# Kernel tuning notes

Measured on AMD Instinct MI355X. Metric: run time of the kernel, lower is better.

The kernel has to match this reference:

```python
import jax, jax.numpy as jnp
import numpy as np

WS = 7   # window size (square)
SS = 3   # shift size
NH = 4   # num heads


def build_rel_index(ws):
    # relative_position_index, identical to the torch buffer construction
    coords = np.stack(np.meshgrid(np.arange(ws), np.arange(ws), indexing='ij'))  # (2, ws, ws)
    flat = coords.reshape(2, -1)                       # (2, ws*ws)
    rel = flat[:, :, None] - flat[:, None, :]          # (2, N, N)
    rel = rel.transpose(1, 2, 0).copy()                # (N, N, 2)
    rel[:, :, 0] += ws - 1
    rel[:, :, 1] += ws - 1
    rel[:, :, 0] *= 2 * ws - 1
    return rel.sum(-1)                                 # (N, N) int


def build_shift_mask(Hp, Wp, ws, ss):
    # additive mask (nW, N, N) with 0 / -100, same as compute_mask
    img = np.zeros((Hp, Wp))
    cnt = 0
    for hs in (slice(0, -ws), slice(-ws, -ss), slice(-ss, None)):
        for wsl in (slice(0, -ws), slice(-ws, -ss), slice(-ss, None)):
            img[hs, wsl] = cnt
            cnt += 1
    mw = img.reshape(Hp // ws, ws, Wp // ws, ws).transpose(0, 2, 1, 3).reshape(-1, ws * ws)
    diff = mw[:, None, :] - mw[:, :, None]
    return jnp.asarray(np.where(diff != 0, -100.0, 0.0).astype(np.float32))


def setup_inputs() -> dict:
    key = jax.random.key(0)
    k1, k2, k3, k4 = jax.random.split(key, 4)
    B, H, W, C = 32, 56, 56, 128
    x = jax.random.normal(k1, (B, H, W, C), dtype=jnp.float32)
    rpb_table = jax.random.normal(k2, ((2 * WS - 1) * (2 * WS - 1), NH), dtype=jnp.float32) * 0.02
    w_qkv = jax.random.normal(k3, (3 * C, C), dtype=jnp.float32) * 0.02
    w_proj = jax.random.normal(k4, (C, C), dtype=jnp.float32) * 0.02
    b_proj = jnp.zeros((C,), dtype=jnp.float32)
    return {"x": x, "rpb_table": rpb_table, "w_qkv": w_qkv, "w_proj": w_proj, "b_proj": b_proj}


def reference(x, rpb_table, w_qkv, w_proj, b_proj):
    B, H, W, C = x.shape
    hd = C // NH
    scale = hd ** (-0.5)
    # pad to multiples of window (no-op for 56x56 / 7)
    pad_b = (-H) % WS
    pad_r = (-W) % WS
    x = jnp.pad(x, ((0, 0), (0, pad_b), (0, pad_r), (0, 0)))
    Hp, Wp = H + pad_b, W + pad_r
    # cyclic shift
    xs = jnp.roll(x, (-SS, -SS), axis=(1, 2))
    nWh, nWw = Hp // WS, Wp // WS
    N = WS * WS
    nW = nWh * nWw
    # window partition -> (B*nW, N, C)
    win = xs.reshape(B, nWh, WS, nWw, WS, C).transpose(0, 1, 3, 2, 4, 5).reshape(-1, N, C)
    # qkv projection (no bias)
    qkv = (win @ w_qkv.T).reshape(-1, N, 3, NH, hd)
    q = qkv[:, :, 0].transpose(0, 2, 1, 3) * scale   # (B_, NH, N, hd)
    k = qkv[:, :, 1].transpose(0, 2, 1, 3)
    v = qkv[:, :, 2].transpose(0, 2, 1, 3)
    attn = jnp.einsum('bhid,bhjd->bhij', q, k)       # (B_, NH, N, N)
    # relative position bias gather
    rel_idx = build_rel_index(WS)                    # (N, N) static
    bias = rpb_table[rel_idx.reshape(-1)].reshape(N, N, NH).transpose(2, 0, 1)
    attn = attn + bias[None]
    # shift mask (shift > 0 since H,W > window)
    mask = build_shift_mask(Hp, Wp, WS, SS)          # (nW, N, N)
    attn = attn.reshape(B, nW, NH, N, N) + mask[None, :, None]
    attn = jax.nn.softmax(attn.reshape(-1, NH, N, N), axis=-1)
    out = jnp.einsum('bhij,bhjd->bihd', attn, v).reshape(-1, N, C)
    out = out @ w_proj.T + b_proj
    # window reverse (square windows -> equivalent to torch code)
    out = out.reshape(B, nWh, nWw, WS, WS, C).transpose(0, 1, 3, 2, 4, 5).reshape(B, Hp, Wp, C)
    out = jnp.roll(out, (SS, SS), axis=(1, 2))
    return out[:, :H, :W, :]
```

## Files before the change

### kernel.cpp

```cpp
#include <hip/hip_runtime.h>


#define HWD 56
#define SCALE_Q 0.17677669529663687f

typedef _Float16 f16x8 __attribute__((ext_vector_type(8)));
typedef __fp16   h16x2 __attribute__((ext_vector_type(2)));
typedef float    f32x4 __attribute__((ext_vector_type(4)));

__device__ __forceinline__ unsigned pkrtz(float a, float b) {
    union { h16x2 h; unsigned u; } r;
    r.h = __builtin_amdgcn_cvt_pkrtz(a, b);
    return r.u;
}

__device__ __forceinline__ f32x4 mfma16(const unsigned a[4], const unsigned b[4], f32x4 c) {
    union { unsigned u[4]; f16x8 h; } A, B;
    A.u[0] = a[0]; A.u[1] = a[1]; A.u[2] = a[2]; A.u[3] = a[3];
    B.u[0] = b[0]; B.u[1] = b[1]; B.u[2] = b[2]; B.u[3] = b[3];
    return __builtin_amdgcn_mfma_f32_16x16x32_f16(A.h, B.h, c, 0, 0, 0);
}

__device__ __forceinline__ unsigned short f16b(float v) {
    union { _Float16 h; unsigned short s; } cv; cv.h = (_Float16)v; return cv.s;
}

__global__ void prep2(const float* __restrict__ rpb,
                      const float* __restrict__ w_qkv,
                      const float* __restrict__ w_proj,
                      unsigned short* __restrict__ whQKV,
                      unsigned short* __restrict__ whP,
                      float* __restrict__ biasT)
{
    int idx = blockIdx.x * 256 + threadIdx.x;
    if (idx < 49152) {
        float v = w_qkv[idx];
        if (idx < 16384) v *= SCALE_Q;
        whQKV[idx] = f16b(v);
    } else if (idx < 65536) {
        int j = idx - 49152;
        whP[j] = f16b(w_proj[j]);
    } else {
        int k = idx - 65536;
        int j = k & 63, i = (k >> 6) & 63, h = (k >> 12) & 3, t = k >> 14;
        float v;
        if (j >= 49)      v = -1e30f;
        else if (i >= 49) v = 0.f;
        else {
            int ri = i / 7, ci = i % 7, rj = j / 7, cj = j % 7;
            int rel = (ri - rj + 6) * 13 + (ci - cj + 6);
            v = rpb[rel * 4 + h];
            int gi = ((t & 2) ? (ri < 4 ? 1 : 2) : 0) * 3 + ((t & 1) ? (ci < 4 ? 1 : 2) : 0);
            int gj = ((t & 2) ? (rj < 4 ? 1 : 2) : 0) * 3 + ((t & 1) ? (cj < 4 ? 1 : 2) : 0);
            if (gi != gj) v -= 100.f;
        }
        biasT[k] = v;
    }
}

__global__ __launch_bounds__(256, 3)
void swin_msa_mfma6(const float* __restrict__ x,
                    const unsigned short* __restrict__ whQKV,
                    const unsigned short* __restrict__ whP,
                    const float* __restrict__ b_proj,
                    const float* __restrict__ biasT,
                    float* __restrict__ out)
{
    __shared__ __align__(16) unsigned short Xs[64 * 136];
    __shared__ __align__(16) unsigned short Osh[64 * 136];

    const int tid  = threadIdx.x;
    const int h    = tid >> 6;
    const int lane = tid & 63;
    const int c    = lane & 15;
    const int g    = lane >> 4;

    const int blk  = blockIdx.x;
    const int b    = blk >> 6;
    const int wIdx = blk & 63;
    const int wh   = wIdx >> 3, ww = wIdx & 7;
    const int wtype = ((wh == 7) ? 2 : 0) | ((ww == 7) ? 1 : 0);

    auto tokAddr = [&](int tok) {
        int rr = tok / 7, cc = tok - rr * 7;
        int sh = wh * 7 + rr + 3; if (sh >= HWD) sh -= HWD;
        int sw = ww * 7 + cc + 3; if (sw >= HWD) sw -= HWD;
        return ((b * HWD + sh) * HWD + sw) * 128;
    };

    for (int idx = tid; idx < 2048; idx += 256) {
        int tok = idx >> 5, ch4 = (idx & 31) << 2;
        uint2 wv = make_uint2(0u, 0u);
        if (tok < 49) {
            const float4 v = *(const float4*)(x + tokAddr(tok) + ch4);
            wv = make_uint2(pkrtz(v.x, v.y), pkrtz(v.z, v.w));
        }
        *(uint2*)&Xs[tok * 136 + ch4] = wv;
    }
    __syncthreads();

    const int srcA  = c | ((lane & 16) << 1);
    const int srcB  = srcA + 16;
    const bool hiSel = (lane & 32) != 0;

    auto redist = [&](const unsigned pkLo[2], const unsigned pkHi[2], unsigned f[4]) {
        #pragma unroll
        for (int p = 0; p < 2; ++p) {
            unsigned lo0 = __shfl(pkLo[p], srcA);
            unsigned hi0 = __shfl(pkHi[p], srcA);
            f[p] = hiSel ? hi0 : lo0;
            unsigned lo1 = __shfl(pkLo[p], srcB);
            unsigned hi1 = __shfl(pkHi[p], srcB);
            f[2 + p] = hiSel ? hi1 : lo1;
        }
    };
    auto loadW = [&](const unsigned short* wbase, int rowBase, unsigned af[4][4]) {
        const unsigned short* wr = wbase + (rowBase + c) * 128 + g * 8;
        #pragma unroll
        for (int kk = 0; kk < 4; ++kk) {
            uint4 v = *(const uint4*)(wr + kk * 32);
            af[kk][0] = v.x; af[kk][1] = v.y; af[kk][2] = v.z; af[kk][3] = v.w;
        }
    };
    auto xfrag = [&](int nt, unsigned xB[4][4]) {
        const unsigned short* xr = &Xs[(nt * 16 + c) * 136 + g * 8];
        #pragma unroll
        for (int kk = 0; kk < 4; ++kk) {
            uint4 v = *(const uint4*)(xr + kk * 32);
            xB[kk][0] = v.x; xB[kk][1] = v.y; xB[kk][2] = v.z; xB[kk][3] = v.w;
        }
    };

    unsigned qB[4][4];
    unsigned kA[4][4];
    unsigned vA[2][2][4];
    {
        unsigned pkP[2][4][2];
        #pragma unroll
        for (int ql = 0; ql < 2; ++ql) {
            unsigned af[4][4];
            loadW(whQKV, 32 * h + 16 * ql, af);
            #pragma unroll
            for (int nt = 0; nt < 4; ++nt) {
                unsigned xB[4][4]; xfrag(nt, xB);
                f32x4 acc = {0.f, 0.f, 0.f, 0.f};
                #pragma unroll
                for (int kk = 0; kk < 4; ++kk) acc = mfma16(af[kk], xB[kk], acc);
                pkP[ql][nt][0] = pkrtz(acc[0], acc[1]);
                pkP[ql][nt][1] = pkrtz(acc[2], acc[3]);
            }
        }
        #pragma unroll
        for (int nt = 0; nt < 4; ++nt) redist(pkP[0][nt], pkP[1][nt], qB[nt]);

        #pragma unroll
        for (int kl = 0; kl < 2; ++kl) {
            unsigned af[4][4];
            loadW(whQKV, 128 + 32 * h + 16 * kl, af);
            #pragma unroll
            for (int mt = 0; mt < 4; ++mt) {
                unsigned xB[4][4]; xfrag(mt, xB);
                f32x4 acc = {0.f, 0.f, 0.f, 0.f};
                #pragma unroll
                for (int kk = 0; kk < 4; ++kk) acc = mfma16(af[kk], xB[kk], acc);
                pkP[kl][mt][0] = pkrtz(acc[0], acc[1]);
                pkP[kl][mt][1] = pkrtz(acc[2], acc[3]);
            }
        }
        #pragma unroll
        for (int mt = 0; mt < 4; ++mt) redist(pkP[0][mt], pkP[1][mt], kA[mt]);
    }
    #pragma unroll
    for (int vl = 0; vl < 2; ++vl) {
        unsigned bf[4][4];
        loadW(whQKV, 256 + 32 * h + 16 * vl, bf);
        unsigned pkV[4][2];
        #pragma unroll
        for (int mt = 0; mt < 4; ++mt) {
            unsigned xA[4][4]; xfrag(mt, xA);
            f32x4 acc = {0.f, 0.f, 0.f, 0.f};
            #pragma unroll
            for (int kk = 0; kk < 4; ++kk) acc = mfma16(xA[kk], bf[kk], acc);
            pkV[mt][0] = pkrtz(acc[0], acc[1]);
            pkV[mt][1] = pkrtz(acc[2], acc[3]);
        }
        #pragma unroll
        for (int kv = 0; kv < 2; ++kv)
            redist(pkV[2 * kv], pkV[2 * kv + 1], vA[vl][kv]);
    }

    const float* bT = biasT + (wtype * 4 + h) * 4096;

    #pragma unroll
    for (int nt = 0; nt < 4; ++nt) {
        f32x4 S[4];
        #pragma unroll
        for (int mt = 0; mt < 4; ++mt) {
            float4 b4 = *(const float4*)&bT[(nt * 16 + c) * 64 + mt * 16 + 4 * g];
            f32x4 C = { b4.x, b4.y, b4.z, b4.w };
            S[mt] = mfma16(kA[mt], qB[nt], C);
        }
        float m = -1e30f;
        #pragma unroll
        for (int mt = 0; mt < 4; ++mt)
            #pragma unroll
            for (int r = 0; r < 4; ++r) m = fmaxf(m, S[mt][r]);
        m = fmaxf(m, __shfl_xor(m, 16));
        m = fmaxf(m, __shfl_xor(m, 32));
        float s = 0.f;
        #pragma unroll
        for (int mt = 0; mt < 4; ++mt)
            #pragma unroll
            for (int r = 0; r < 4; ++r) { float e = __expf(S[mt][r] - m); S[mt][r] = e; s += e; }
        s += __shfl_xor(s, 16);
        s += __shfl_xor(s, 32);
        const float iv = 1.0f / s;

        f32x4 o0 = {0.f, 0.f, 0.f, 0.f};
        f32x4 o1 = {0.f, 0.f, 0.f, 0.f};
        #pragma unroll
        for (int kk = 0; kk < 2; ++kk) {
            unsigned pkLo[2], pkHi[2];
            pkLo[0] = pkrtz(S[2 * kk][0] * iv,     S[2 * kk][1] * iv);
            pkLo[1] = pkrtz(S[2 * kk][2] * iv,     S[2 * kk][3] * iv);
            pkHi[0] = pkrtz(S[2 * kk + 1][0] * iv, S[2 * kk + 1][1] * iv);
            pkHi[1] = pkrtz(S[2 * kk + 1][2] * iv, S[2 * kk + 1][3] * iv);
            unsigned pB[4];
            redist(pkLo, pkHi, pB);
            o0 = mfma16(vA[0][kk], pB, o0);
            o1 = mfma16(vA[1][kk], pB, o1);
        }
        *(uint2*)&Osh[(nt * 16 + c) * 136 + 32 * h + 4 * g] =
            make_uint2(pkrtz(o0[0], o0[1]), pkrtz(o0[2], o0[3]));
        *(uint2*)&Osh[(nt * 16 + c) * 136 + 32 * h + 16 + 4 * g] =
            make_uint2(pkrtz(o1[0], o1[1]), pkrtz(o1[2], o1[3]));
    }
    __syncthreads();

    int taddr[4];
    #pragma unroll
    for (int nt = 0; nt < 4; ++nt) {
        int tok = nt * 16 + c;
        taddr[nt] = (tok < 49) ? tokAddr(tok) : -1;
    }
    unsigned oB[4][4][4];
    #pragma unroll
    for (int nt = 0; nt < 4; ++nt)
        #pragma unroll
        for (int kk = 0; kk < 4; ++kk) {
            uint4 v = *(const uint4*)&Osh[(nt * 16 + c) * 136 + kk * 32 + g * 8];
            oB[nt][kk][0] = v.x; oB[nt][kk][1] = v.y; oB[nt][kk][2] = v.z; oB[nt][kk][3] = v.w;
        }
    #pragma unroll
    for (int mi = 0; mi < 2; ++mi) {
        const int mt = 2 * h + mi;
        unsigned aW[4][4];
        loadW(whP, 16 * mt, aW);
        float4 bias4 = *(const float4*)(b_proj + mt * 16 + 4 * g);
        #pragma unroll
        for (int nt = 0; nt < 4; ++nt) {
            f32x4 acc = {0.f, 0.f, 0.f, 0.f};
            #pragma unroll
            for (int kk = 0; kk < 4; ++kk) acc = mfma16(aW[kk], oB[nt][kk], acc);
            if (taddr[nt] >= 0) {
                float4 o = make_float4(acc[0] + bias4.x, acc[1] + bias4.y,
                                       acc[2] + bias4.z, acc[3] + bias4.w);
                *(float4*)(out + taddr[nt] + mt * 16 + 4 * g) = o;
            }
        }
    }
}

extern "C" void kernel_launch(void* const* d_in, const int* in_sizes, int n_in,
                              void* d_out, int out_size, void* d_ws, size_t ws_size,
                              hipStream_t stream) {
    const float* x     = (const float*)d_in[0];
    const float* rpb   = (const float*)d_in[1];
    const float* wqkv  = (const float*)d_in[2];
    const float* wproj = (const float*)d_in[3];
    const float* bproj = (const float*)d_in[4];
    float* outp = (float*)d_out;

    unsigned short* whQKV = (unsigned short*)d_ws;
    unsigned short* whP   = whQKV + 49152;
    float* biasT = (float*)(whP + 16384);

    prep2<<<512, 256, 0, stream>>>(rpb, wqkv, wproj, whQKV, whP, biasT);
    swin_msa_mfma6<<<32 * 64, 256, 0, stream>>>(x, whQKV, whP, bproj, biasT, outp);
}
```

Baseline: 68.95 us.

## Process each window with a single wavefront looping over all heads

Result: slower. 86.93 us (+26.1%).

```diff
diff --git a/kernel.cpp b/kernel.cpp
--- a/kernel.cpp
+++ b/kernel.cpp
@@ -58,20 +58,17 @@
     }
 }
 
-__global__ __launch_bounds__(256, 3)
-void swin_msa_mfma6(const float* __restrict__ x,
-                    const unsigned short* __restrict__ whQKV,
-                    const unsigned short* __restrict__ whP,
-                    const float* __restrict__ b_proj,
-                    const float* __restrict__ biasT,
-                    float* __restrict__ out)
+__global__ __launch_bounds__(64, 3)
+void swin_msa_win1(const float* __restrict__ x,
+                   const unsigned short* __restrict__ whQKV,
+                   const unsigned short* __restrict__ whP,
+                   const float* __restrict__ b_proj,
+                   const float* __restrict__ biasT,
+                   float* __restrict__ out)
 {
     __shared__ __align__(16) unsigned short Xs[64 * 136];
-    __shared__ __align__(16) unsigned short Osh[64 * 136];
-
-    const int tid  = threadIdx.x;
-    const int h    = tid >> 6;
-    const int lane = tid & 63;
+
+    const int lane = threadIdx.x;
     const int c    = lane & 15;
     const int g    = lane >> 4;
 
@@ -88,7 +85,7 @@
         return ((b * HWD + sh) * HWD + sw) * 128;
     };
 
-    for (int idx = tid; idx < 2048; idx += 256) {
+    for (int idx = lane; idx < 2048; idx += 64) {
         int tok = idx >> 5, ch4 = (idx & 31) << 2;
         uint2 wv = make_uint2(0u, 0u);
         if (tok < 49) {
@@ -97,7 +94,6 @@
         }
         *(uint2*)&Xs[tok * 136 + ch4] = wv;
     }
-    __syncthreads();
 
     const int srcA  = c | ((lane & 16) << 1);
     const int srcB  = srcA + 16;
@@ -131,111 +127,111 @@
         }
     };
 
-    unsigned qB[4][4];
-    unsigned kA[4][4];
-    unsigned vA[2][2][4];
-    {
-        unsigned pkP[2][4][2];
-        #pragma unroll
-        for (int ql = 0; ql < 2; ++ql) {
-            unsigned af[4][4];
-            loadW(whQKV, 32 * h + 16 * ql, af);
-            #pragma unroll
-            for (int nt = 0; nt < 4; ++nt) {
-                unsigned xB[4][4]; xfrag(nt, xB);
+    unsigned oB[4][4][4];
+
+    #pragma unroll
+    for (int h = 0; h < 4; ++h) {
+        unsigned qB[4][4], kA[4][4], vA[2][2][4];
+        {
+            unsigned pkP[2][4][2];
+            #pragma unroll
+            for (int ql = 0; ql < 2; ++ql) {
+                unsigned af[4][4];
+                loadW(whQKV, 32 * h + 16 * ql, af);
+                #pragma unroll
+                for (int nt = 0; nt < 4; ++nt) {
+                    unsigned xB[4][4]; xfrag(nt, xB);
+                    f32x4 acc = {0.f, 0.f, 0.f, 0.f};
+                    #pragma unroll
+                    for (int kk = 0; kk < 4; ++kk) acc = mfma16(af[kk], xB[kk], acc);
+                    pkP[ql][nt][0] = pkrtz(acc[0], acc[1]);
+                    pkP[ql][nt][1] = pkrtz(acc[2], acc[3]);
+                }
+            }
+            #pragma unroll
+            for (int nt = 0; nt < 4; ++nt) redist(pkP[0][nt], pkP[1][nt], qB[nt]);
+
+            #pragma unroll
+            for (int kl = 0; kl < 2; ++kl) {
+                unsigned af[4][4];
+                loadW(whQKV, 128 + 32 * h + 16 * kl, af);
+                #pragma unroll
+                for (int mt = 0; mt < 4; ++mt) {
+                    unsigned xB[4][4]; xfrag(mt, xB);
+                    f32x4 acc = {0.f, 0.f, 0.f, 0.f};
+                    #pragma unroll
+                    for (int kk = 0; kk < 4; ++kk) acc = mfma16(af[kk], xB[kk], acc);
+                    pkP[kl][mt][0] = pkrtz(acc[0], acc[1]);
+                    pkP[kl][mt][1] = pkrtz(acc[2], acc[3]);
+                }
+            }
+            #pragma unroll
+            for (int mt = 0; mt < 4; ++mt) redist(pkP[0][mt], pkP[1][mt], kA[mt]);
+        }
+        #pragma unroll
+        for (int vl = 0; vl < 2; ++vl) {
+            unsigned bf[4][4];
+            loadW(whQKV, 256 + 32 * h + 16 * vl, bf);
+            unsigned pkV[4][2];
+            #pragma unroll
+            for (int mt = 0; mt < 4; ++mt) {
+                unsigned xA[4][4]; xfrag(mt, xA);
                 f32x4 acc = {0.f, 0.f, 0.f, 0.f};
                 #pragma unroll
-                for (int kk = 0; kk < 4; ++kk) acc = mfma16(af[kk], xB[kk], acc);
-                pkP[ql][nt][0] = pkrtz(acc[0], acc[1]);
-                pkP[ql][nt][1] = pkrtz(acc[2], acc[3]);
-            }
-        }
-        #pragma unroll
-        for (int nt = 0; nt < 4; ++nt) redist(pkP[0][nt], pkP[1][nt], qB[nt]);
-
-        #pragma unroll
-        for (int kl = 0; kl < 2; ++kl) {
-            unsigned af[4][4];
-            loadW(whQKV, 128 + 32 * h + 16 * kl, af);
+                for (int kk = 0; kk < 4; ++kk) acc = mfma16(xA[kk], bf[kk], acc);
+                pkV[mt][0] = pkrtz(acc[0], acc[1]);
+                pkV[mt][1] = pkrtz(acc[2], acc[3]);
+            }
+            #pragma unroll
+            for (int kv = 0; kv < 2; ++kv)
+                redist(pkV[2 * kv], pkV[2 * kv + 1], vA[vl][kv]);
+        }
+
+        const float* bT = biasT + (wtype * 4 + h) * 4096;
+        #pragma unroll
+        for (int nt = 0; nt < 4; ++nt) {
+            f32x4 S[4];
             #pragma unroll
             for (int mt = 0; mt < 4; ++mt) {
-                unsigned xB[4][4]; xfrag(mt, xB);
-                f32x4 acc = {0.f, 0.f, 0.f, 0.f};
-                #pragma unroll
-                for (int kk = 0; kk < 4; ++kk) acc = mfma16(af[kk], xB[kk], acc);
-                pkP[kl][mt][0] = pkrtz(acc[0], acc[1]);
-                pkP[kl][mt][1] = pkrtz(acc[2], acc[3]);
-            }
-        }
-        #pragma unroll
-        for (int mt = 0; mt < 4; ++mt) redist(pkP[0][mt], pkP[1][mt], kA[mt]);
-    }
-    #pragma unroll
-    for (int vl = 0; vl < 2; ++vl) {
-        unsigned bf[4][4];
-        loadW(whQKV, 256 + 32 * h + 16 * vl, bf);
-        unsigned pkV[4][2];
-        #pragma unroll
-        for (int mt = 0; mt < 4; ++mt) {
-            unsigned xA[4][4]; xfrag(mt, xA);
-            f32x4 acc = {0.f, 0.f, 0.f, 0.f};
-            #pragma unroll
-            for (int kk = 0; kk < 4; ++kk) acc = mfma16(xA[kk], bf[kk], acc);
-            pkV[mt][0] = pkrtz(acc[0], acc[1]);
-            pkV[mt][1] = pkrtz(acc[2], acc[3]);
-        }
-        #pragma unroll
-        for (int kv = 0; kv < 2; ++kv)
-            redist(pkV[2 * kv], pkV[2 * kv + 1], vA[vl][kv]);
-    }
-
-    const float* bT = biasT + (wtype * 4 + h) * 4096;
-
-    #pragma unroll
-    for (int nt = 0; nt < 4; ++nt) {
-        f32x4 S[4];
-        #pragma unroll
-        for (int mt = 0; mt < 4; ++mt) {
-            float4 b4 = *(const float4*)&bT[(nt * 16 + c) * 64 + mt * 16 + 4 * g];
-            f32x4 C = { b4.x, b4.y, b4.z, b4.w };
-            S[mt] = mfma16(kA[mt], qB[nt], C);
-        }
-        float m = -1e30f;
-        #pragma unroll
-        for (int mt = 0; mt < 4; ++mt)
-            #pragma unroll
-            for (int r = 0; r < 4; ++r) m = fmaxf(m, S[mt][r]);
-        m = fmaxf(m, __shfl_xor(m, 16));
-        m = fmaxf(m, __shfl_xor(m, 32));
-        float s = 0.f;
-        #pragma unroll
-        for (int mt = 0; mt < 4; ++mt)
-            #pragma unroll
-            for (int r = 0; r < 4; ++r) { float e = __expf(S[mt][r] - m); S[mt][r] = e; s += e; }
-        s += __shfl_xor(s, 16);
-        s += __shfl_xor(s, 32);
-        const float iv = 1.0f / s;
-
-        f32x4 o0 = {0.f, 0.f, 0.f, 0.f};
-        f32x4 o1 = {0.f, 0.f, 0.f, 0.f};
-        #pragma unroll
-        for (int kk = 0; kk < 2; ++kk) {
-            unsigned pkLo[2], pkHi[2];
-            pkLo[0] = pkrtz(S[2 * kk][0] * iv,     S[2 * kk][1] * iv);
-            pkLo[1] = pkrtz(S[2 * kk][2] * iv,     S[2 * kk][3] * iv);
-            pkHi[0] = pkrtz(S[2 * kk + 1][0] * iv, S[2 * kk + 1][1] * iv);
-            pkHi[1] = pkrtz(S[2 * kk + 1][2] * iv, S[2 * kk + 1][3] * iv);
-            unsigned pB[4];
-            redist(pkLo, pkHi, pB);
-            o0 = mfma16(vA[0][kk], pB, o0);
-            o1 = mfma16(vA[1][kk], pB, o1);
-        }
-        *(uint2*)&Osh[(nt * 16 + c) * 136 + 32 * h + 4 * g] =
-            make_uint2(pkrtz(o0[0], o0[1]), pkrtz(o0[2], o0[3]));
-        *(uint2*)&Osh[(nt * 16 + c) * 136 + 32 * h + 16 + 4 * g] =
-            make_uint2(pkrtz(o1[0], o1[1]), pkrtz(o1[2], o1[3]));
-    }
-    __syncthreads();
+                float4 b4 = *(const float4*)&bT[(nt * 16 + c) * 64 + mt * 16 + 4 * g];
+                f32x4 C = { b4.x, b4.y, b4.z, b4.w };
+                S[mt] = mfma16(kA[mt], qB[nt], C);
+            }
+            float m = -1e30f;
+            #pragma unroll
+            for (int mt = 0; mt < 4; ++mt)
+                #pragma unroll
+                for (int r = 0; r < 4; ++r) m = fmaxf(m, S[mt][r]);
+            m = fmaxf(m, __shfl_xor(m, 16));
+            m = fmaxf(m, __shfl_xor(m, 32));
+            float s = 0.f;
+            #pragma unroll
+            for (int mt = 0; mt < 4; ++mt)
+                #pragma unroll
+                for (int r = 0; r < 4; ++r) { float e = __expf(S[mt][r] - m); S[mt][r] = e; s += e; }
+            s += __shfl_xor(s, 16);
+            s += __shfl_xor(s, 32);
+            const float iv = 1.0f / s;
+
+            f32x4 o0 = {0.f, 0.f, 0.f, 0.f};
+            f32x4 o1 = {0.f, 0.f, 0.f, 0.f};
+            #pragma unroll
+            for (int kk = 0; kk < 2; ++kk) {
+                unsigned pkLo[2], pkHi[2];
+                pkLo[0] = pkrtz(S[2 * kk][0] * iv,     S[2 * kk][1] * iv);
+                pkLo[1] = pkrtz(S[2 * kk][2] * iv,     S[2 * kk][3] * iv);
+                pkHi[0] = pkrtz(S[2 * kk + 1][0] * iv, S[2 * kk + 1][1] * iv);
+                pkHi[1] = pkrtz(S[2 * kk + 1][2] * iv, S[2 * kk + 1][3] * iv);
+                unsigned pB[4];
+                redist(pkLo, pkHi, pB);
+                o0 = mfma16(vA[0][kk], pB, o0);
+                o1 = mfma16(vA[1][kk], pB, o1);
+            }
+            unsigned OpkLo[2] = { pkrtz(o0[0], o0[1]), pkrtz(o0[2], o0[3]) };
+            unsigned OpkHi[2] = { pkrtz(o1[0], o1[1]), pkrtz(o1[2], o1[3]) };
+            redist(OpkLo, OpkHi, oB[h][nt]);
+        }
+    }
 
     int taddr[4];
     #pragma unroll
@@ -243,17 +239,8 @@
         int tok = nt * 16 + c;
         taddr[nt] = (tok < 49) ? tokAddr(tok) : -1;
     }
-    unsigned oB[4][4][4];
     #pragma unroll
-    for (int nt = 0; nt < 4; ++nt)
-        #pragma unroll
-        for (int kk = 0; kk < 4; ++kk) {
-            uint4 v = *(const uint4*)&Osh[(nt * 16 + c) * 136 + kk * 32 + g * 8];
-            oB[nt][kk][0] = v.x; oB[nt][kk][1] = v.y; oB[nt][kk][2] = v.z; oB[nt][kk][3] = v.w;
-        }
-    #pragma unroll
-    for (int mi = 0; mi < 2; ++mi) {
-        const int mt = 2 * h + mi;
+    for (int mt = 0; mt < 8; ++mt) {
         unsigned aW[4][4];
         loadW(whP, 16 * mt, aW);
         float4 bias4 = *(const float4*)(b_proj + mt * 16 + 4 * g);
@@ -261,7 +248,7 @@
         for (int nt = 0; nt < 4; ++nt) {
             f32x4 acc = {0.f, 0.f, 0.f, 0.f};
             #pragma unroll
-            for (int kk = 0; kk < 4; ++kk) acc = mfma16(aW[kk], oB[nt][kk], acc);
+            for (int kk = 0; kk < 4; ++kk) acc = mfma16(aW[kk], oB[kk][nt], acc);
             if (taddr[nt] >= 0) {
                 float4 o = make_float4(acc[0] + bias4.x, acc[1] + bias4.y,
                                        acc[2] + bias4.z, acc[3] + bias4.w);
@@ -286,5 +273,5 @@
     float* biasT = (float*)(whP + 16384);
 
     prep2<<<512, 256, 0, stream>>>(rpb, wqkv, wproj, whQKV, whP, biasT);
-    swin_msa_mfma6<<<32 * 64, 256, 0, stream>>>(x, whQKV, whP, bproj, biasT, outp);
-}
+    swin_msa_win1<<<2048, 64, 0, stream>>>(x, whQKV, whP, bproj, biasT, outp);
+}
```
